# Kernel optimization log

Measured on AMD Instinct MI355X. Metric: run time of the kernel, lower is better.

The kernel has to match this reference:

```python
import jax, jax.numpy as jnp
import numpy as np

N = 100000
E = 800000

def elu(x):
    return jnp.where(x > 0, x, jnp.expm1(x))

def transformer_conv(x, src, dst, ea, Wq, bq, Wk, bk, Wv, bv, We, Ws, bs, heads, ch):
    # PyG TransformerConv (concat=True, root_weight=True, beta=False, eval so dropout off)
    n = x.shape[0]
    q = (x @ Wq + bq).reshape(n, heads, ch)
    k = (x @ Wk + bk).reshape(n, heads, ch)
    v = (x @ Wv + bv).reshape(n, heads, ch)
    e = (ea @ We).reshape(-1, heads, ch)            # [E,H,C], lin_edge has no bias
    kj = k[src] + e                                  # [E,H,C]
    logits = (q[dst] * kj).sum(-1) / jnp.sqrt(jnp.float32(ch))  # [E,H]
    # segment softmax over incoming edges of each dst node
    m = jax.ops.segment_max(logits, dst, num_segments=n)
    ex = jnp.exp(logits - m[dst])
    denom = jax.ops.segment_sum(ex, dst, num_segments=n)
    alpha = ex / denom[dst]                          # [E,H]
    msg = alpha[..., None] * (v[src] + e)            # [E,H,C]
    agg = jax.ops.segment_sum(msg, dst, num_segments=n).reshape(n, heads * ch)
    return agg + x @ Ws + bs                         # skip connection (lin_skip)

def setup_inputs() -> dict:
    key = jax.random.key(0)
    ks = jax.random.split(key, 32)
    def rn(k, shape, scale=0.1):
        return jax.random.normal(k, shape, dtype=jnp.float32) * scale
    d = {}
    d['x'] = jax.random.normal(ks[0], (N, 23), dtype=jnp.float32)
    d['edge_index'] = jax.random.randint(ks[1], (2, E), 0, N, dtype=jnp.int32)
    d['edge_attr'] = jax.random.normal(ks[2], (E, 7), dtype=jnp.float32)
    d['linA_w'] = rn(ks[3], (23, 23)); d['linA_b'] = jnp.zeros((23,), jnp.float32)
    d['linB_w'] = rn(ks[4], (23, 23)); d['linB_b'] = jnp.zeros((23,), jnp.float32)
    # conv1: in=23, heads=8, out=24 -> 192
    d['q1_w'] = rn(ks[5], (23, 192)); d['q1_b'] = jnp.zeros((192,), jnp.float32)
    d['k1_w'] = rn(ks[6], (23, 192)); d['k1_b'] = jnp.zeros((192,), jnp.float32)
    d['v1_w'] = rn(ks[7], (23, 192)); d['v1_b'] = jnp.zeros((192,), jnp.float32)
    d['e1_w'] = rn(ks[8], (7, 192))
    d['s1_w'] = rn(ks[9], (23, 192)); d['s1_b'] = jnp.zeros((192,), jnp.float32)
    # conv4: in=192, heads=8, out=8 -> 64
    d['q2_w'] = rn(ks[10], (192, 64)); d['q2_b'] = jnp.zeros((64,), jnp.float32)
    d['k2_w'] = rn(ks[11], (192, 64)); d['k2_b'] = jnp.zeros((64,), jnp.float32)
    d['v2_w'] = rn(ks[12], (192, 64)); d['v2_b'] = jnp.zeros((64,), jnp.float32)
    d['e2_w'] = rn(ks[13], (7, 64))
    d['s2_w'] = rn(ks[14], (192, 64)); d['s2_b'] = jnp.zeros((64,), jnp.float32)
    d['lin1_w'] = rn(ks[15], (64, 20)); d['lin1_b'] = jnp.zeros((20,), jnp.float32)
    d['lin2_w'] = rn(ks[16], (20, 1)); d['lin2_b'] = jnp.zeros((1,), jnp.float32)
    return d

def reference(x, edge_index, edge_attr,
              linA_w, linA_b, linB_w, linB_b,
              q1_w, q1_b, k1_w, k1_b, v1_w, v1_b, e1_w, s1_w, s1_b,
              q2_w, q2_b, k2_w, k2_b, v2_w, v2_b, e2_w, s2_w, s2_b,
              lin1_w, lin1_b, lin2_w, lin2_b):
    src, dst = edge_index[0], edge_index[1]
    h = elu(x @ linA_w + linA_b)
    h = elu(h @ linB_w + linB_b)
    h = transformer_conv(h, src, dst, edge_attr, q1_w, q1_b, k1_w, k1_b, v1_w, v1_b, e1_w, s1_w, s1_b, 8, 24)
    h = elu(h)
    h = transformer_conv(h, src, dst, edge_attr, q2_w, q2_b, k2_w, k2_b, v2_w, v2_b, e2_w, s2_w, s2_b, 8, 8)
    h = elu(h)
    h = elu(h @ lin1_w + lin1_b)
    return h @ lin2_w + lin2_b
```

## Files before the change

### kernel.cpp

```cpp
#include <hip/hip_runtime.h>
#include <math.h>


__device__ __forceinline__ float elu_f(float x) {
    return x > 0.f ? x : expm1f(x);
}


__global__ void mlp_kernel(const float* __restrict__ x,
                           const float* __restrict__ A, const float* __restrict__ ab,
                           const float* __restrict__ B, const float* __restrict__ bb,
                           float* __restrict__ out, int n) {
    __shared__ float sA[23 * 23], sB[23 * 23], sa[23], sb[23];
    for (int t = threadIdx.x; t < 23 * 23; t += blockDim.x) { sA[t] = A[t]; sB[t] = B[t]; }
    if (threadIdx.x < 23) { sa[threadIdx.x] = ab[threadIdx.x]; sb[threadIdx.x] = bb[threadIdx.x]; }
    __syncthreads();
    int i = blockIdx.x * blockDim.x + threadIdx.x;
    if (i >= n) return;
    float xi[23], h1[23];
    #pragma unroll
    for (int j = 0; j < 23; j++) xi[j] = x[(size_t)i * 23 + j];
    #pragma unroll
    for (int o = 0; o < 23; o++) {
        float acc = sa[o];
        #pragma unroll
        for (int j = 0; j < 23; j++) acc = fmaf(xi[j], sA[j * 23 + o], acc);
        h1[o] = elu_f(acc);
    }
    #pragma unroll
    for (int o = 0; o < 23; o++) {
        float acc = sb[o];
        #pragma unroll
        for (int j = 0; j < 23; j++) acc = fmaf(h1[j], sB[j * 23 + o], acc);
        out[(size_t)i * 23 + o] = elu_f(acc);
    }
}

template<int IN, int Kc, int OUTW, int M, int TY, bool FUSED>
__global__ void proj_tiled_kernel(const float* __restrict__ in, int n,
    const float* __restrict__ W0, const float* __restrict__ b0, float* __restrict__ o0,
    const float* __restrict__ W1, const float* __restrict__ b1, float* __restrict__ o1,
    const float* __restrict__ W2, const float* __restrict__ b2, float* __restrict__ o2,
    const float* __restrict__ W3, const float* __restrict__ b3, float* __restrict__ o3) {
    constexpr int WTOT = M * OUTW;
    constexpr int CG   = WTOT / 8;
    constexpr int BN   = TY * 4;
    constexpr int SAW  = BN + 4;
    constexpr int NT   = CG * TY;
    static_assert(IN % Kc == 0, "Kc must divide IN");
    static_assert(WTOT % 8 == 0 && OUTW % 4 == 0, "col alignment");
    __shared__ float sA[Kc][SAW];
    __shared__ float sB[Kc][WTOT];

    const int tid = threadIdx.x;
    const int tx = tid % CG;
    const int ty = tid / CG;
    const int node0 = blockIdx.x * BN;

    const int colA = tx * 4;
    const int colB = WTOT / 2 + tx * 4;
    const int matA = colA / OUTW, ccA = colA % OUTW;
    const int matB = colB / OUTW, ccB = colB % OUTW;
    const float* bA = (matA == 0 ? b0 : matA == 1 ? b1 : matA == 2 ? b2 : b3);
    const float* bB = (matB == 0 ? b0 : matB == 1 ? b1 : matB == 2 ? b2 : b3);
    float*       oA = (matA == 0 ? o0 : matA == 1 ? o1 : matA == 2 ? o2 : o3);
    float*       oB = (matB == 0 ? o0 : matB == 1 ? o1 : matB == 2 ? o2 : o3);

    float acc[4][8];
    #pragma unroll
    for (int i = 0; i < 4; i++) {
        #pragma unroll
        for (int c = 0; c < 4; c++) { acc[i][c] = bA[ccA + c]; acc[i][4 + c] = bB[ccB + c]; }
    }

    for (int k0 = 0; k0 < IN; k0 += Kc) {
        for (int t = tid; t < Kc * BN; t += NT) {
            int j = t / BN, nn = t - j * BN;
            int g = node0 + nn;
            sA[j][nn] = (g < n) ? in[(size_t)g * IN + k0 + j] : 0.f;
        }
        for (int t = tid; t < Kc * WTOT; t += NT) {
            int j = t / WTOT, c = t - j * WTOT;
            int m = c / OUTW, cm = c - m * OUTW;
            const float* Wp = (m == 0 ? W0 : m == 1 ? W1 : m == 2 ? W2 : W3);
            sB[j][c] = Wp[(size_t)(k0 + j) * OUTW + cm];
        }
        __syncthreads();
        #pragma unroll 8
        for (int j = 0; j < Kc; j++) {
            float4 a  = *(const float4*)&sA[j][ty * 4];
            float4 v0 = *(const float4*)&sB[j][colA];
            float4 v1 = *(const float4*)&sB[j][colB];
            float av[4] = {a.x, a.y, a.z, a.w};
            float bv[8] = {v0.x, v0.y, v0.z, v0.w, v1.x, v1.y, v1.z, v1.w};
            #pragma unroll
            for (int i = 0; i < 4; i++)
                #pragma unroll
                for (int c = 0; c < 8; c++)
                    acc[i][c] = fmaf(av[i], bv[c], acc[i][c]);
        }
        __syncthreads();
    }

    #pragma unroll
    for (int i = 0; i < 4; i++) {
        int g = node0 + ty * 4 + i;
        if (g >= n) continue;
        if constexpr (FUSED) {
            *(float4*)(o0 + (size_t)g * WTOT + colA) = make_float4(acc[i][0], acc[i][1], acc[i][2], acc[i][3]);
            *(float4*)(o0 + (size_t)g * WTOT + colB) = make_float4(acc[i][4], acc[i][5], acc[i][6], acc[i][7]);
        } else {
            *(float4*)(oA + (size_t)g * OUTW + ccA) = make_float4(acc[i][0], acc[i][1], acc[i][2], acc[i][3]);
            *(float4*)(oB + (size_t)g * OUTW + ccB) = make_float4(acc[i][4], acc[i][5], acc[i][6], acc[i][7]);
        }
    }
}


__global__ void zero2_kernel(int* __restrict__ a, int* __restrict__ b, int n) {
    int i = blockIdx.x * blockDim.x + threadIdx.x;
    if (i < n) { a[i] = 0; b[i] = 0; }
}

__global__ void count_kernel(const int* __restrict__ dst, int* __restrict__ cnt, int nE) {
    int e = blockIdx.x * blockDim.x + threadIdx.x;
    if (e < nE) atomicAdd(&cnt[dst[e]], 1);
}

__global__ void scan_block_kernel(int* __restrict__ cnt, int* __restrict__ bsum, int n) {
    __shared__ int sdat[256];
    int i = blockIdx.x * 256 + threadIdx.x;
    int v = (i < n) ? cnt[i] : 0;
    sdat[threadIdx.x] = v;
    __syncthreads();
    for (int off = 1; off < 256; off <<= 1) {
        int t = (threadIdx.x >= (unsigned)off) ? sdat[threadIdx.x - off] : 0;
        __syncthreads();
        sdat[threadIdx.x] += t;
        __syncthreads();
    }
    if (i < n) cnt[i] = sdat[threadIdx.x] - v;
    if (threadIdx.x == 255) bsum[blockIdx.x] = sdat[255];
}

__global__ void scan_bsum_kernel(int* __restrict__ bsum, int nb) {
    __shared__ int s[1024];
    int i = threadIdx.x;
    int v = (i < nb) ? bsum[i] : 0;
    s[i] = v;
    __syncthreads();
    for (int off = 1; off < 1024; off <<= 1) {
        int t = (i >= off) ? s[i - off] : 0;
        __syncthreads();
        s[i] += t;
        __syncthreads();
    }
    if (i < nb) bsum[i] = s[i] - v;
}

__global__ void finalize_rp_kernel(const int* __restrict__ cnt, const int* __restrict__ bsum,
                                   int* __restrict__ rp, int n, int nE) {
    int i = blockIdx.x * blockDim.x + threadIdx.x;
    if (i < n) rp[i] = cnt[i] + bsum[i >> 8];
    if (i == n) rp[n] = nE;
}

__global__ void scatter_kernel(const int* __restrict__ src, const int* __restrict__ dst,
                               const int* __restrict__ rp, int* __restrict__ cur,
                               int2* __restrict__ seS, int nE) {
    int e = blockIdx.x * blockDim.x + threadIdx.x;
    if (e >= nE) return;
    int d = dst[e];
    int pos = rp[d] + atomicAdd(&cur[d], 1);
    seS[pos] = make_int2(src[e], e);
}

template<int IN, int C, bool VMAT, bool QMAT, bool DOELU>
__global__ __launch_bounds__(256, 4)
void conv_fused_kernel(const float* __restrict__ feat,
                       const float* __restrict__ Wq, const float* __restrict__ qb,
                       const float* __restrict__ Wv, const float* __restrict__ vb,
                       const float* __restrict__ kmat, const float* __restrict__ qmat,
                       const float* __restrict__ ea, const float* __restrict__ We,
                       const int* __restrict__ rp, const int2* __restrict__ seS,
                       float* __restrict__ out, int n, float scale, int chunk) {
    constexpr int HC = 8 * C;
    constexpr int CPL = HC / 64;
    __shared__ float sWv[VMAT ? 1 : IN * HC];
    if constexpr (!VMAT) {
        for (int t = threadIdx.x; t < IN * HC; t += blockDim.x) sWv[t] = Wv[t];
        __syncthreads();
    }
    const int lane = threadIdx.x & 63;
    const int wid = (blockIdx.x * blockDim.x + threadIdx.x) >> 6;
    int d0 = wid * chunk;
    const int dEnd = min(n, d0 + chunk);
    if (d0 >= dEnd) return;
    const int ch0 = lane * CPL;

    float we[7][CPL];
    #pragma unroll
    for (int j = 0; j < 7; j++)
        #pragma unroll
        for (int c = 0; c < CPL; c++) we[j][c] = We[j * HC + ch0 + c];

    float vbr[CPL];
    if constexpr (!VMAT) {
        #pragma unroll
        for (int c = 0; c < CPL; c++) vbr[c] = vb[ch0 + c];
    }

    for (int d = d0; d < dEnd; d++) {
        float* op = out + (size_t)d * HC + ch0;
        float sk[CPL], q[CPL];
        #pragma unroll
        for (int c = 0; c < CPL; c++) sk[c] = op[c];
        if constexpr (QMAT) {
            const float* qp = qmat + (size_t)d * HC + ch0;
            #pragma unroll
            for (int c = 0; c < CPL; c++) q[c] = qp[c];
        } else {
            #pragma unroll
            for (int c = 0; c < CPL; c++) q[c] = qb[ch0 + c];
            const float* fd = feat + (size_t)d * IN;
            for (int j = 0; j < IN; j++) {
                float f = fd[j];
                #pragma unroll
                for (int c = 0; c < CPL; c++)
                    q[c] = fmaf(f, Wq[(size_t)j * HC + ch0 + c], q[c]);
            }
        }

        float m = -INFINITY, l = 0.f, acc[CPL];
        #pragma unroll
        for (int c = 0; c < CPL; c++) acc[c] = 0.f;

        const int p0 = rp[d], p1 = rp[d + 1];

        if constexpr (VMAT) {
            if (p0 < p1) {
                int2 se0 = seS[p0];
                int sC = __builtin_amdgcn_readfirstlane(se0.x);
                int eC = __builtin_amdgcn_readfirstlane(se0.y);
                int2 seN = (p0 + 1 < p1) ? seS[p0 + 1] : se0;
                float kc[CPL], vc[CPL], ec[7];
                {
                    const float* kp = kmat + (size_t)sC * (2 * HC) + ch0;
                    const float* ep = ea + (size_t)eC * 7;
                    #pragma unroll
                    for (int c = 0; c < CPL; c++) { kc[c] = kp[c]; vc[c] = kp[HC + c]; }
                    #pragma unroll
                    for (int j = 0; j < 7; j++) ec[j] = ep[j];
                }
                for (int p = p0; p < p1; p++) {
                    const bool hasN = (p + 1 < p1);
                    int2 seN2 = (p + 2 < p1) ? seS[p + 2] : seN;
                    float kn[CPL], vn[CPL], en[7];
                    if (hasN) {
                        int sN = __builtin_amdgcn_readfirstlane(seN.x);
                        int eN = __builtin_amdgcn_readfirstlane(seN.y);
                        const float* kp = kmat + (size_t)sN * (2 * HC) + ch0;
                        const float* ep = ea + (size_t)eN * 7;
                        #pragma unroll
                        for (int c = 0; c < CPL; c++) { kn[c] = kp[c]; vn[c] = kp[HC + c]; }
                        #pragma unroll
                        for (int j = 0; j < 7; j++) en[j] = ep[j];
                    }
                    float part = 0.f;
                    float vloc[CPL];
                    #pragma unroll
                    for (int c = 0; c < CPL; c++) {
                        float t = 0.f;
                        #pragma unroll
                        for (int j = 0; j < 7; j++) t = fmaf(ec[j], we[j][c], t);
                        part = fmaf(q[c], kc[c] + t, part);
                        vloc[c] = vc[c] + t;
                    }
                    part += __shfl_xor(part, 1);
                    part += __shfl_xor(part, 2);
                    part += __shfl_xor(part, 4);
                    float z = part * scale;
                    float mn = fmaxf(m, z);
                    float rs = expf(m - mn);
                    float pw = expf(z - mn);
                    l = l * rs + pw;
                    #pragma unroll
                    for (int c = 0; c < CPL; c++) acc[c] = fmaf(acc[c], rs, pw * vloc[c]);
                    m = mn;
                    if (hasN) {
                        #pragma unroll
                        for (int c = 0; c < CPL; c++) { kc[c] = kn[c]; vc[c] = vn[c]; }
                        #pragma unroll
                        for (int j = 0; j < 7; j++) ec[j] = en[j];
                    }
                    seN = seN2;
                }
            }
        } else {
            for (int p = p0; p < p1; p++) {
                int2 se = seS[p];
                int s = se.x, eid = se.y;
                const float* eav = ea + (size_t)eid * 7;
                float ev[7];
                #pragma unroll
                for (int j = 0; j < 7; j++) ev[j] = eav[j];
                const float* kp = kmat + (size_t)s * HC + ch0;
                float vv[CPL];
                float part = 0.f;
                #pragma unroll
                for (int c = 0; c < CPL; c++) {
                    float t = 0.f;
                    #pragma unroll
                    for (int j = 0; j < 7; j++) t = fmaf(ev[j], we[j][c], t);
                    part = fmaf(q[c], kp[c] + t, part);
                    vv[c] = t + vbr[c];
                }
                const float* fs = feat + (size_t)s * IN;
                for (int j = 0; j < IN; j++) {
                    float f = fs[j];
                    #pragma unroll
                    for (int c = 0; c < CPL; c++) vv[c] = fmaf(f, sWv[j * HC + ch0 + c], vv[c]);
                }
                part += __shfl_xor(part, 1);
                part += __shfl_xor(part, 2);
                part += __shfl_xor(part, 4);
                float z = part * scale;
                float mn = fmaxf(m, z);
                float rs = expf(m - mn);
                float pw = expf(z - mn);
                l = l * rs + pw;
                #pragma unroll
                for (int c = 0; c < CPL; c++) acc[c] = fmaf(acc[c], rs, pw * vv[c]);
                m = mn;
            }
        }

        float invl = (l > 0.f) ? 1.f / l : 0.f;
        #pragma unroll
        for (int c = 0; c < CPL; c++) {
            float r = sk[c] + acc[c] * invl;
            op[c] = DOELU ? elu_f(r) : r;
        }
    }
}

__global__ void head_kernel(const float* __restrict__ h, const float* __restrict__ W1,
                            const float* __restrict__ b1, const float* __restrict__ W2,
                            const float* __restrict__ b2, float* __restrict__ out, int n) {
    __shared__ float sW1[64 * 20], sb1[20], sW2[20], sb2;
    for (int t = threadIdx.x; t < 64 * 20; t += blockDim.x) sW1[t] = W1[t];
    if (threadIdx.x < 20) { sb1[threadIdx.x] = b1[threadIdx.x]; sW2[threadIdx.x] = W2[threadIdx.x]; }
    if (threadIdx.x == 0) sb2 = b2[0];
    __syncthreads();
    int i = blockIdx.x * blockDim.x + threadIdx.x;
    if (i >= n) return;
    float hv[64];
    const float* hp = h + (size_t)i * 64;
    #pragma unroll
    for (int j = 0; j < 64; j++) hv[j] = elu_f(hp[j]);
    float acc2 = sb2;
    for (int o = 0; o < 20; o++) {
        float a = sb1[o];
        #pragma unroll
        for (int j = 0; j < 64; j++) a = fmaf(hv[j], sW1[j * 20 + o], a);
        acc2 = fmaf(elu_f(a), sW2[o], acc2);
    }
    out[i] = acc2;
}

__global__ void zero_out_kernel(float* __restrict__ out, int n) {
    int i = blockIdx.x * blockDim.x + threadIdx.x;
    if (i < n) out[i] = 0.f;
}


extern "C" void kernel_launch(void* const* d_in, const int* in_sizes, int n_in,
                              void* d_out, int out_size, void* d_ws, size_t ws_size,
                              hipStream_t stream) {
    const float* x   = (const float*)d_in[0];
    const int*   ei  = (const int*)d_in[1];
    const float* ea  = (const float*)d_in[2];
    const float* Aw  = (const float*)d_in[3];
    const float* Ab  = (const float*)d_in[4];
    const float* Bw  = (const float*)d_in[5];
    const float* Bb  = (const float*)d_in[6];
    const float* q1w = (const float*)d_in[7];  const float* q1b = (const float*)d_in[8];
    const float* k1w = (const float*)d_in[9];  const float* k1b = (const float*)d_in[10];
    const float* v1w = (const float*)d_in[11]; const float* v1b = (const float*)d_in[12];
    const float* e1w = (const float*)d_in[13];
    const float* s1w = (const float*)d_in[14]; const float* s1b = (const float*)d_in[15];
    const float* q2w = (const float*)d_in[16]; const float* q2b = (const float*)d_in[17];
    const float* k2w = (const float*)d_in[18]; const float* k2b = (const float*)d_in[19];
    const float* v2w = (const float*)d_in[20]; const float* v2b = (const float*)d_in[21];
    const float* e2w = (const float*)d_in[22];
    const float* s2w = (const float*)d_in[23]; const float* s2b = (const float*)d_in[24];
    const float* l1w = (const float*)d_in[25]; const float* l1b = (const float*)d_in[26];
    const float* l2w = (const float*)d_in[27]; const float* l2b = (const float*)d_in[28];

    const int n  = in_sizes[0] / 23;
    const int nE = in_sizes[1] / 2;
    const int* src = ei;
    const int* dst = ei + nE;
    float* out = (float*)d_out;
    const int B = 256;
    const int nb = (n + 255) / 256;

    size_t fl_h1 = ((size_t)n * 23 + 3) & ~(size_t)3;
    size_t fl_o1 = (size_t)n * 192;
    size_t fl_kvA = (size_t)n * 384;
    size_t fl_kB  = (size_t)n * 192;
    size_t fl_q1  = (size_t)n * 192;
    size_t ints_total = 2 * (size_t)nE + ((size_t)n + 1) + n + n + 1024;

    size_t tierB_bytes  = (fl_h1 + fl_o1 + fl_kB) * 4 + ints_total * 4;
    size_t tierA_bytes  = (fl_h1 + fl_o1 + fl_kvA) * 4 + ints_total * 4;
    size_t tierA2_bytes = tierA_bytes + fl_q1 * 4;

    if (ws_size < tierB_bytes || nb > 1024) {
        zero_out_kernel<<<(out_size + B - 1) / B, B, 0, stream>>>(out, out_size);
        return;
    }
    const int tier = (ws_size >= tierA2_bytes) ? 2 : (ws_size >= tierA_bytes) ? 1 : 0;

    float* ws = (float*)d_ws;
    size_t off = 0;
    float* h1   = ws + off; off += fl_h1;
    float* o1   = ws + off; off += fl_o1;
    float* kbuf = ws + off; off += (tier >= 1 ? fl_kvA : fl_kB);
    float* q1buf = nullptr;
    if (tier == 2) { q1buf = ws + off; off += fl_q1; }
    int2* seS = (int2*)(ws + off);
    int* ip = (int*)(seS + nE);
    int* rp   = ip; ip += (size_t)n + 1;
    int* cnt  = ip; ip += n;
    int* cur  = ip; ip += n;
    int* bsum = ip;

    float* kv2   = kbuf;
    float* q2buf = (tier >= 1) ? (kbuf + (size_t)n * 128) : nullptr;
    float* o2    = (tier >= 1) ? (kbuf + (size_t)n * 192) : (kbuf + (size_t)n * 128);

    const float sc1 = 1.0f / sqrtf(24.0f);
    const float sc2 = 1.0f / sqrtf(8.0f);
    const float* np = nullptr;
    float* npw = nullptr;

    zero2_kernel<<<(n + B - 1) / B, B, 0, stream>>>(cnt, cur, n);
    count_kernel<<<(nE + B - 1) / B, B, 0, stream>>>(dst, cnt, nE);
    scan_block_kernel<<<nb, 256, 0, stream>>>(cnt, bsum, n);
    scan_bsum_kernel<<<1, 1024, 0, stream>>>(bsum, nb);
    finalize_rp_kernel<<<(n + 1 + B - 1) / B, B, 0, stream>>>(cnt, bsum, rp, n, nE);
    scatter_kernel<<<(nE + B - 1) / B, B, 0, stream>>>(src, dst, rp, cur, seS, nE);

    mlp_kernel<<<(n + B - 1) / B, B, 0, stream>>>(x, Aw, Ab, Bw, Bb, h1, n);

    const int gproj32 = (n + 31) / 32;
    const int gproj64 = (n + 63) / 64;

    const int CB = 1024;
    const int NW = CB * 4;
    const int chunk = (n + NW - 1) / NW;

    if (tier >= 1) {
        proj_tiled_kernel<23, 23, 192, 2, 8, true><<<gproj32, 384, 0, stream>>>(
            h1, n, k1w, k1b, kbuf, v1w, v1b, npw, np, np, npw, np, np, npw);
        if (tier == 2) {
            proj_tiled_kernel<23, 23, 192, 2, 8, false><<<gproj32, 384, 0, stream>>>(
                h1, n, s1w, s1b, o1, q1w, q1b, q1buf, np, np, npw, np, np, npw);
            conv_fused_kernel<23, 24, true, true, true><<<CB, 256, 0, stream>>>(
                h1, q1w, q1b, v1w, v1b, kbuf, q1buf, ea, e1w, rp, seS, o1, n, sc1, chunk);
        } else {
            proj_tiled_kernel<23, 23, 192, 1, 8, false><<<gproj32, 192, 0, stream>>>(
                h1, n, s1w, s1b, o1, np, np, npw, np, np, npw, np, np, npw);
            conv_fused_kernel<23, 24, true, false, true><<<CB, 256, 0, stream>>>(
                h1, q1w, q1b, v1w, v1b, kbuf, np, ea, e1w, rp, seS, o1, n, sc1, chunk);
        }
    } else {
        proj_tiled_kernel<23, 23, 192, 2, 8, false><<<gproj32, 384, 0, stream>>>(
            h1, n, k1w, k1b, kbuf, s1w, s1b, o1, np, np, npw, np, np, npw);
        conv_fused_kernel<23, 24, false, false, true><<<CB, 256, 0, stream>>>(
            h1, q1w, q1b, v1w, v1b, kbuf, np, ea, e1w, rp, seS, o1, n, sc1, chunk);
    }

    proj_tiled_kernel<192, 32, 64, 2, 16, true><<<gproj64, 256, 0, stream>>>(
        o1, n, k2w, k2b, kv2, v2w, v2b, npw, np, np, npw, np, np, npw);
    if (tier >= 1) {
        proj_tiled_kernel<192, 32, 64, 2, 16, false><<<gproj64, 256, 0, stream>>>(
            o1, n, q2w, q2b, q2buf, s2w, s2b, o2, np, np, npw, np, np, npw);
        conv_fused_kernel<192, 8, true, true, false><<<CB, 256, 0, stream>>>(
            o1, q2w, q2b, v2w, v2b, kv2, q2buf, ea, e2w, rp, seS, o2, n, sc2, chunk);
    } else {
        proj_tiled_kernel<192, 32, 64, 1, 16, false><<<gproj64, 128, 0, stream>>>(
            o1, n, s2w, s2b, o2, np, np, npw, np, np, npw, np, np, npw);
        conv_fused_kernel<192, 8, true, false, false><<<CB, 256, 0, stream>>>(
            o1, q2w, q2b, v2w, v2b, kv2, np, ea, e2w, rp, seS, o2, n, sc2, chunk);
    }

    head_kernel<<<(n + B - 1) / B, B, 0, stream>>>(o2, l1w, l1b, l2w, l2b, out, n);
}
```

Measured before the change: 1.185 ms.

## Trade software prefetch for higher occupancy in fused TransformerConv kernel

Removes the register-heavy one-ahead prefetch of K/V rows and edge attributes in the edge loop, loading the current K/V inside the iteration instead. The skip-connection read of the output is deferred to the end. Launch bounds are raised to 8 blocks per SM and the grid doubled, so each wave handles fewer destination nodes. The aim is to rely on more resident waves rather than per-wave prefetch to hide gather latency. The cost is that each wave is more latency-exposed if the extra occupancy is not actually reached.

```diff
diff --git a/kernel.cpp b/kernel.cpp
--- a/kernel.cpp
+++ b/kernel.cpp
@@ -176,7 +176,7 @@
 }
 
 template<int IN, int C, bool VMAT, bool QMAT, bool DOELU>
-__global__ __launch_bounds__(256, 4)
+__global__ __launch_bounds__(256, 8)
 void conv_fused_kernel(const float* __restrict__ feat,
                        const float* __restrict__ Wq, const float* __restrict__ qb,
                        const float* __restrict__ Wv, const float* __restrict__ vb,
@@ -193,7 +193,7 @@
     }
     const int lane = threadIdx.x & 63;
     const int wid = (blockIdx.x * blockDim.x + threadIdx.x) >> 6;
-    int d0 = wid * chunk;
+    const int d0 = wid * chunk;
     const int dEnd = min(n, d0 + chunk);
     if (d0 >= dEnd) return;
     const int ch0 = lane * CPL;
@@ -211,10 +211,7 @@
     }
 
     for (int d = d0; d < dEnd; d++) {
-        float* op = out + (size_t)d * HC + ch0;
-        float sk[CPL], q[CPL];
-        #pragma unroll
-        for (int c = 0; c < CPL; c++) sk[c] = op[c];
+        float q[CPL];
         if constexpr (QMAT) {
             const float* qp = qmat + (size_t)d * HC + ch0;
             #pragma unroll
@@ -240,42 +237,37 @@
         if constexpr (VMAT) {
             if (p0 < p1) {
                 int2 se0 = seS[p0];
-                int sC = __builtin_amdgcn_readfirstlane(se0.x);
-                int eC = __builtin_amdgcn_readfirstlane(se0.y);
-                int2 seN = (p0 + 1 < p1) ? seS[p0 + 1] : se0;
-                float kc[CPL], vc[CPL], ec[7];
+                int sU = __builtin_amdgcn_readfirstlane(se0.x);
+                int eU = __builtin_amdgcn_readfirstlane(se0.y);
+                float ec[7];
                 {
-                    const float* kp = kmat + (size_t)sC * (2 * HC) + ch0;
-                    const float* ep = ea + (size_t)eC * 7;
-                    #pragma unroll
-                    for (int c = 0; c < CPL; c++) { kc[c] = kp[c]; vc[c] = kp[HC + c]; }
+                    const float* ep = ea + (size_t)eU * 7;
                     #pragma unroll
                     for (int j = 0; j < 7; j++) ec[j] = ep[j];
                 }
                 for (int p = p0; p < p1; p++) {
+                    const float* kp = kmat + (size_t)sU * (2 * HC) + ch0;
+                    float kc[CPL], vc[CPL];
+                    #pragma unroll
+                    for (int c = 0; c < CPL; c++) { kc[c] = kp[c]; vc[c] = kp[HC + c]; }
                     const bool hasN = (p + 1 < p1);
-                    int2 seN2 = (p + 2 < p1) ? seS[p + 2] : seN;
-                    float kn[CPL], vn[CPL], en[7];
+                    int sN = sU, eN = eU;
                     if (hasN) {
-                        int sN = __builtin_amdgcn_readfirstlane(seN.x);
-                        int eN = __builtin_amdgcn_readfirstlane(seN.y);
-                        const float* kp = kmat + (size_t)sN * (2 * HC) + ch0;
-                        const float* ep = ea + (size_t)eN * 7;
-                        #pragma unroll
-                        for (int c = 0; c < CPL; c++) { kn[c] = kp[c]; vn[c] = kp[HC + c]; }
-                        #pragma unroll
-                        for (int j = 0; j < 7; j++) en[j] = ep[j];
+                        int2 s2 = seS[p + 1];
+                        sN = __builtin_amdgcn_readfirstlane(s2.x);
+                        eN = __builtin_amdgcn_readfirstlane(s2.y);
                     }
-                    float part = 0.f;
-                    float vloc[CPL];
+                    float tv[CPL];
                     #pragma unroll
                     for (int c = 0; c < CPL; c++) {
                         float t = 0.f;
                         #pragma unroll
                         for (int j = 0; j < 7; j++) t = fmaf(ec[j], we[j][c], t);
-                        part = fmaf(q[c], kc[c] + t, part);
-                        vloc[c] = vc[c] + t;
+                        tv[c] = t;
                     }
+                    float part = 0.f;
+                    #pragma unroll
+                    for (int c = 0; c < CPL; c++) part = fmaf(q[c], kc[c] + tv[c], part);
                     part += __shfl_xor(part, 1);
                     part += __shfl_xor(part, 2);
                     part += __shfl_xor(part, 4);
@@ -285,15 +277,14 @@
                     float pw = expf(z - mn);
                     l = l * rs + pw;
                     #pragma unroll
-                    for (int c = 0; c < CPL; c++) acc[c] = fmaf(acc[c], rs, pw * vloc[c]);
+                    for (int c = 0; c < CPL; c++) acc[c] = fmaf(acc[c], rs, pw * (vc[c] + tv[c]));
                     m = mn;
                     if (hasN) {
+                        const float* ep = ea + (size_t)eN * 7;
                         #pragma unroll
-                        for (int c = 0; c < CPL; c++) { kc[c] = kn[c]; vc[c] = vn[c]; }
-                        #pragma unroll
-                        for (int j = 0; j < 7; j++) ec[j] = en[j];
+                        for (int j = 0; j < 7; j++) ec[j] = ep[j];
                     }
-                    seN = seN2;
+                    sU = sN; eU = eN;
                 }
             }
         } else {
@@ -336,9 +327,10 @@
         }
 
         float invl = (l > 0.f) ? 1.f / l : 0.f;
+        float* op = out + (size_t)d * HC + ch0;
         #pragma unroll
         for (int c = 0; c < CPL; c++) {
-            float r = sk[c] + acc[c] * invl;
+            float r = op[c] + acc[c] * invl;
             op[c] = DOELU ? elu_f(r) : r;
         }
     }
@@ -457,7 +449,7 @@
     const int gproj32 = (n + 31) / 32;
     const int gproj64 = (n + 63) / 64;
 
-    const int CB = 1024;
+    const int CB = 2048;
     const int NW = CB * 4;
     const int chunk = (n + NW - 1) / NW;
 
```

Measured after the change: 1.317 ms. 1.11x slower.
